# Optimization experiments

Hardware: AMD Instinct MI355X
Metric: run time of the kernel (lower is better)

Reference implementation:

```python
import jax, jax.numpy as jnp
import numpy as np

N = 50000
E = 1600000
HID = 128
H = 8
D = HID // H


def _layer_norm(x, g, b, eps=1e-5):
    mu = jnp.mean(x, axis=-1, keepdims=True)
    var = jnp.mean(jnp.square(x - mu), axis=-1, keepdims=True)
    return (x - mu) * jax.lax.rsqrt(var + eps) * g + b


def setup_inputs() -> dict:
    key = jax.random.key(0)
    ks = jax.random.split(key, 20)
    s = 1.0 / np.sqrt(HID)
    inp = {
        "x": jax.random.normal(ks[0], (N, HID), jnp.float32),
        "edge_index": jax.random.randint(ks[1], (2, E), 0, N, jnp.int64),
        "edge_attr": jax.random.randint(ks[2], (E,), 0, 13, jnp.int64),
        # projections (stored as [in, out] so y = x @ W + b)
        "Wq": jax.random.normal(ks[3], (HID, HID), jnp.float32) * s,
        "bq": jnp.zeros((HID,), jnp.float32),
        "Wk": jax.random.normal(ks[4], (HID, HID), jnp.float32) * s,
        "bk": jnp.zeros((HID,), jnp.float32),
        "Wv": jax.random.normal(ks[5], (HID, HID), jnp.float32) * s,
        "bv": jnp.zeros((HID,), jnp.float32),
        "Wo": jax.random.normal(ks[6], (HID, HID), jnp.float32) * s,
        "bo": jnp.zeros((HID,), jnp.float32),
        "edge_bias_table": jax.random.normal(ks[7], (13, H), jnp.float32) * 0.02,
        "W1": jax.random.normal(ks[8], (HID, 4 * HID), jnp.float32) * s,
        "b1": jnp.zeros((4 * HID,), jnp.float32),
        "W2": jax.random.normal(ks[9], (4 * HID, HID), jnp.float32) * (0.5 * s),
        "b2": jnp.zeros((HID,), jnp.float32),
        "g1": jnp.ones((HID,), jnp.float32),
        "be1": jnp.zeros((HID,), jnp.float32),
        "g2": jnp.ones((HID,), jnp.float32),
        "be2": jnp.zeros((HID,), jnp.float32),
    }
    return inp


def reference(x, edge_index, edge_attr, Wq, bq, Wk, bk, Wv, bv, Wo, bo,
              edge_bias_table, W1, b1, W2, b2, g1, be1, g2, be2):
    n = x.shape[0]
    residual = x
    h = _layer_norm(x, g1, be1)
    Q = (h @ Wq + bq).reshape(n, H, D)
    K = (h @ Wk + bk).reshape(n, H, D)
    V = (h @ Wv + bv).reshape(n, H, D)
    src, dst = edge_index[0], edge_index[1]
    # per-edge scores [E, H]
    scores = jnp.sum(Q[dst] * K[src], axis=-1) / np.sqrt(D)
    scores = scores + edge_bias_table[jnp.clip(edge_attr, 0, 12)]
    # scatter softmax over incoming edges of each dst (global max, as in source)
    scores_exp = jnp.exp(scores - jnp.max(scores))
    attn_sum = jax.ops.segment_sum(scores_exp, dst, num_segments=n)  # [N, H]
    attn_w = scores_exp / (attn_sum[dst] + 1e-8)                      # [E, H]
    messages = V[src] * attn_w[..., None]                             # [E, H, D]
    out = jax.ops.segment_sum(messages, dst, num_segments=n)          # [N, H, D]
    out = out.reshape(n, HID) @ Wo + bo
    x = residual + out  # dropout is identity in eval
    residual = x
    h2 = _layer_norm(x, g2, be2)
    ffn = jax.nn.relu(h2 @ W1 + b1) @ W2 + b2
    return residual + ffn
```

## Files before the change

### kernel.cpp

```cpp
#include <hip/hip_runtime.h>
#include <hip/hip_bf16.h>

#define N_NODES 50000
#define E_EDGES 1600000
#define HID 128
#define NH 8
#define HD 16

#define NBKT 196
#define BKT_CAP 9216
#define CHUNK_A 4096
#define EPT 16
#define BINA_BLOCKS ((E_EDGES + CHUNK_A - 1) / CHUNK_A)
#define WCVT_BLOCKS 771
#define LN_BLOCKS 12500
#define QKV_XBLOCKS ((N_NODES + 127) / 128)
#define ATTN_BLOCKS 2048

using short8 = __attribute__((ext_vector_type(8))) short;
using f32x4  = __attribute__((ext_vector_type(4))) float;
using f32x2  = __attribute__((ext_vector_type(2))) float;
typedef _Float16 h16x2 __attribute__((ext_vector_type(2)));

#if defined(__has_builtin) && __has_builtin(__builtin_amdgcn_fdot2)
#define FDOT2(a, b, c) __builtin_amdgcn_fdot2((a), (b), (c), false)
#else
__device__ __forceinline__ float FDOT2(h16x2 a, h16x2 b, float c) {
    return fmaf((float)a[0], (float)b[0], fmaf((float)a[1], (float)b[1], c));
}
#endif

__device__ __forceinline__ float wave_reduce_sum(float v) {
    #pragma unroll
    for (int off = 32; off > 0; off >>= 1) v += __shfl_xor(v, off, 64);
    return v;
}

__device__ __forceinline__ unsigned int packbf2(float a, float b) {
    __hip_bfloat162 t;
    t.x = __float2bfloat16(a);
    t.y = __float2bfloat16(b);
    unsigned int u;
    __builtin_memcpy(&u, &t, 4);
    return u;
}

__device__ __forceinline__ unsigned char fp8e(float v) {
    return (unsigned char)(__builtin_amdgcn_cvt_pk_fp8_f32(v, v, 0u, false) & 0xFFu);
}

union U4H {
    uint4 u;
    h16x2 h[4];
};

struct KV {
    U4H k0, k1;
    uint4 v;
};

__device__ __forceinline__ KV loadkv(const char* khs, const unsigned char* v8s, unsigned pk) {
    KV r;
    unsigned rr = pk & 0xFFFFu;
    r.k0.u = *(const uint4*)(khs + (rr << 8));
    r.k1.u = *(const uint4*)(khs + (rr << 8) + 16u);
    r.v = *(const uint4*)(v8s + (rr << 7));
    return r;
}

__device__ __forceinline__ void consume_kv(const KV& kv, unsigned pk, bool vd,
                                           const U4H& q0, const U4H& q1,
                                           const float* bLDS, int sub,
                                           f32x2* acc2, float& wsum) {
    float p = 0.f;
    #pragma unroll
    for (int j = 0; j < 4; ++j) p = FDOT2(q0.h[j], kv.k0.h[j], p);
    #pragma unroll
    for (int j = 0; j < 4; ++j) p = FDOT2(q1.h[j], kv.k1.h[j], p);
    float s = p + bLDS[((pk >> 16) & 0xFu) * 8 + sub];
    float w = vd ? __expf(s) : 0.f;
    wsum += w;
    f32x2 w2; w2[0] = w; w2[1] = w;
    f32x2 t;
    t = __builtin_amdgcn_cvt_pk_f32_fp8(kv.v.x, false); acc2[0] = t * w2 + acc2[0];
    t = __builtin_amdgcn_cvt_pk_f32_fp8(kv.v.x, true);  acc2[1] = t * w2 + acc2[1];
    t = __builtin_amdgcn_cvt_pk_f32_fp8(kv.v.y, false); acc2[2] = t * w2 + acc2[2];
    t = __builtin_amdgcn_cvt_pk_f32_fp8(kv.v.y, true);  acc2[3] = t * w2 + acc2[3];
    t = __builtin_amdgcn_cvt_pk_f32_fp8(kv.v.z, false); acc2[4] = t * w2 + acc2[4];
    t = __builtin_amdgcn_cvt_pk_f32_fp8(kv.v.z, true);  acc2[5] = t * w2 + acc2[5];
    t = __builtin_amdgcn_cvt_pk_f32_fp8(kv.v.w, false); acc2[6] = t * w2 + acc2[6];
    t = __builtin_amdgcn_cvt_pk_f32_fp8(kv.v.w, true);  acc2[7] = t * w2 + acc2[7];
}

__global__ __launch_bounds__(256) void prep_kernel(
    const int* __restrict__ ei, const int* __restrict__ attr,
    int* __restrict__ bcur, unsigned int* __restrict__ temp,
    const float* __restrict__ Wq, const float* __restrict__ Wk,
    const float* __restrict__ Wv, const float* __restrict__ Wo,
    const float* __restrict__ W1, const float* __restrict__ W2,
    const float* __restrict__ bq, const float* __restrict__ bk,
    const float* __restrict__ bv,
    __hip_bfloat16* __restrict__ Wqkvt, __hip_bfloat16* __restrict__ Wot,
    __hip_bfloat16* __restrict__ W1t, __hip_bfloat16* __restrict__ W2t,
    float* __restrict__ bqkv,
    const float* __restrict__ x, const float* __restrict__ g1,
    const float* __restrict__ be1, __hip_bfloat16* __restrict__ h_out) {
    __shared__ unsigned int sval[CHUNK_A];
    __shared__ unsigned short sbkt[CHUNK_A];
    __shared__ int hist[NBKT];
    __shared__ int lofs[NBKT];
    __shared__ int gbase[NBKT];
    __shared__ int lcur[NBKT];
    __shared__ int sc[256];
    const int b = blockIdx.x;
    const int tid = threadIdx.x;
    if (b < BINA_BLOCKS) {
        const int e0 = b * CHUNK_A;
        const int n = min(CHUNK_A, E_EDGES - e0);
        for (int i = tid; i < NBKT; i += 256) hist[i] = 0;
        __syncthreads();
        unsigned int v[EPT];
        short bk_[EPT];
        #pragma unroll
        for (int j = 0; j < EPT; ++j) {
            int i = tid + j * 256;
            bk_[j] = -1;
            v[j] = 0;
            if (i < n) {
                int e = e0 + i;
                int src = ei[e];
                int dst = ei[E_EDGES + e];
                int a = attr[e]; a = min(max(a, 0), 12);
                v[j] = (unsigned)src | ((unsigned)a << 16) | ((unsigned)(dst & 255) << 20);
                int bb = dst >> 8;
                bk_[j] = (short)bb;
                atomicAdd(&hist[bb], 1);
            }
        }
        __syncthreads();
        sc[tid] = (tid < NBKT) ? hist[tid] : 0;
        __syncthreads();
        for (int off = 1; off < 256; off <<= 1) {
            int xx = (tid >= off) ? sc[tid - off] : 0;
            __syncthreads();
            sc[tid] += xx;
            __syncthreads();
        }
        if (tid < NBKT) {
            int h = hist[tid];
            lofs[tid] = sc[tid] - h;
            lcur[tid] = 0;
            gbase[tid] = h ? atomicAdd(&bcur[tid], h) : 0;
        }
        __syncthreads();
        #pragma unroll
        for (int j = 0; j < EPT; ++j) {
            if (bk_[j] >= 0) {
                int p = lofs[bk_[j]] + atomicAdd(&lcur[bk_[j]], 1);
                sval[p] = v[j];
                sbkt[p] = (unsigned short)bk_[j];
            }
        }
        __syncthreads();
        for (int i = tid; i < n; i += 256) {
            int bb = sbkt[i];
            temp[(size_t)bb * BKT_CAP + gbase[bb] + (i - lofs[bb])] = sval[i];
        }
    } else if (b < BINA_BLOCKS + WCVT_BLOCKS) {
        int t = (b - BINA_BLOCKS) * 256 + tid;
        if (t >= 196608) {
            int i = t - 196608;
            if (i < 384) bqkv[i] = i < 128 ? bq[i] : (i < 256 ? bk[i - 128] : bv[i - 256]);
            return;
        }
        const float* W; __hip_bfloat16* Wt; int K, N, idx;
        if (t < 65536) {
            int which = t >> 14; idx = t & 16383; K = 128; N = 128;
            W = which == 0 ? Wq : which == 1 ? Wk : which == 2 ? Wv : Wo;
            Wt = which == 3 ? Wot : Wqkvt + which * 16384;
        } else if (t < 131072) { idx = t - 65536;  K = 128; N = 512; W = W1; Wt = W1t; }
        else                   { idx = t - 131072; K = 512; N = 128; W = W2; Wt = W2t; }
        int n = idx / K, k = idx - n * K;
        Wt[idx] = __float2bfloat16(W[(size_t)k * N + n]);
    } else {
        int wave = tid >> 6;
        int lane = tid & 63;
        int row = (b - BINA_BLOCKS - WCVT_BLOCKS) * 4 + wave;
        if (row >= N_NODES) return;
        float2 v = ((const float2*)(x + (size_t)row * HID))[lane];
        float s = wave_reduce_sum(v.x + v.y);
        float mu = s * (1.0f / HID);
        float dx = v.x - mu, dy = v.y - mu;
        float q = wave_reduce_sum(dx * dx + dy * dy);
        float rstd = rsqrtf(q * (1.0f / HID) + 1e-5f);
        float2 gg = ((const float2*)g1)[lane];
        float2 bb = ((const float2*)be1)[lane];
        __hip_bfloat162 o;
        o.x = __float2bfloat16(dx * rstd * gg.x + bb.x);
        o.y = __float2bfloat16(dy * rstd * gg.y + bb.y);
        ((__hip_bfloat162*)(h_out + (size_t)row * HID))[lane] = o;
    }
}

__global__ __launch_bounds__(512) void qkv_binb_kernel(
    const int* __restrict__ bcur, const unsigned int* __restrict__ temp,
    unsigned int* __restrict__ packed, int* __restrict__ offs,
    const __hip_bfloat16* __restrict__ A, const __hip_bfloat16* __restrict__ Wt,
    const float* __restrict__ bias,
    _Float16* __restrict__ Chh, unsigned char* __restrict__ C8, int M) {
    __shared__ short8 smem[2048 + 2048];
    const int tid = threadIdx.x;
    if (blockIdx.x < NBKT) {
        int* cnts = (int*)smem;
        int* hist = cnts + 256;
        int* cur = hist + 256;
        const int b = blockIdx.x;
        if (tid < 256) {
            cnts[tid] = (tid < NBKT) ? bcur[tid] : 0;
            hist[tid] = 0;
        }
        __syncthreads();
        for (int off = 1; off < 256; off <<= 1) {
            int x = 0;
            if (tid < 256 && tid >= off) x = cnts[tid - off];
            __syncthreads();
            if (tid < 256) cnts[tid] += x;
            __syncthreads();
        }
        const int cnt = bcur[b];
        const int start = cnts[b] - cnt;
        const size_t base = (size_t)b * BKT_CAP;
        for (int i = tid; i < cnt; i += 512)
            atomicAdd(&hist[(temp[base + i] >> 20) & 255], 1);
        __syncthreads();
        if (tid < 256) cur[tid] = hist[tid];
        __syncthreads();
        for (int off = 1; off < 256; off <<= 1) {
            int x = 0;
            if (tid < 256 && tid >= off) x = cur[tid - off];
            __syncthreads();
            if (tid < 256) cur[tid] += x;
            __syncthreads();
        }
        const int node0 = b * 256;
        if (tid < 256) {
            int excl = cur[tid] - hist[tid];
            cur[tid] = excl;
            int node = node0 + tid;
            if (node < N_NODES) offs[node] = start + excl;
        }
        if (b == NBKT - 1 && tid == 0) offs[N_NODES] = start + cnt;
        __syncthreads();
        for (int i = tid; i < cnt; i += 512) {
            unsigned int v = temp[base + i];
            int d = (v >> 20) & 255;
            int p = start + atomicAdd(&cur[d], 1);
            packed[p] = v & 0xFFFFFu;
        }
        return;
    }
    const int gb = blockIdx.x - NBKT;
    const int plane = gb / QKV_XBLOCKS;
    const int xb = gb - plane * QKV_XBLOCKS;
    const int row0 = xb * 128;
    const int col0 = plane * 128;
    const int w = tid >> 6, l = tid & 63;
    const int lr = l & 15, hi = l >> 4;
    f32x4 acc[8] = {};
    #pragma unroll
    for (int it = 0; it < 4; ++it) {
        unsigned d = tid + it * 512;
        int r = d >> 4, sd = d & 15;
        int ss = sd ^ (r & 7);
        int gr = row0 + r; if (gr >= M) gr = M - 1;
        __builtin_amdgcn_global_load_lds(
            (const __attribute__((address_space(1))) void*)(A + (size_t)gr * 128 + ss * 8),
            (__attribute__((address_space(3))) void*)(smem + (d & ~63u)),
            16, 0, 0);
    }
    #pragma unroll
    for (int it = 0; it < 4; ++it) {
        unsigned d = tid + it * 512;
        int r = d >> 4, sd = d & 15;
        int ss = sd ^ (r & 7);
        __builtin_amdgcn_global_load_lds(
            (const __attribute__((address_space(1))) void*)(Wt + (size_t)(col0 + r) * 128 + ss * 8),
            (__attribute__((address_space(3))) void*)(smem + 2048 + (d & ~63u)),
            16, 0, 0);
    }
    __syncthreads();
    const int ar = w * 16 + lr;
    #pragma unroll
    for (int ks = 0; ks < 4; ++ks) {
        int s = ks * 4 + hi;
        short8 a = smem[ar * 16 + (s ^ (ar & 7))];
        #pragma unroll
        for (int f = 0; f < 8; ++f) {
            int br = f * 16 + lr;
            short8 b = smem[2048 + br * 16 + (s ^ (br & 7))];
            acc[f] = __builtin_amdgcn_mfma_f32_16x16x32_bf16(a, b, acc[f], 0, 0, 0);
        }
    }
    const float scl = (plane == 0) ? 0.25f : 1.0f;
    #pragma unroll
    for (int f = 0; f < 8; ++f) {
        int c = col0 + f * 16 + lr;
        float bv = bias[c];
        #pragma unroll
        for (int j = 0; j < 4; ++j) {
            int r = row0 + w * 16 + hi * 4 + j;
            if (r < M) {
                float v = acc[f][j] + bv;
                if (plane < 2)
                    Chh[(size_t)plane * N_NODES * 128 + (size_t)r * 128 + (c & 127)] =
                        (_Float16)(v * scl);
                else
                    C8[(size_t)r * 128 + (c & 127)] = fp8e(v);
            }
        }
    }
}

template <int K, int OB>
__global__ __launch_bounds__(512) void gemm_mfma(const __hip_bfloat16* __restrict__ A,
                                                 const __hip_bfloat16* __restrict__ Wt,
                                                 const float* __restrict__ bias,
                                                 const float* __restrict__ res,
                                                 const __hip_bfloat16* __restrict__ resb,
                                                 float* __restrict__ C,
                                                 __hip_bfloat16* __restrict__ Cb,
                                                 __hip_bfloat16* __restrict__ Cx,
                                                 const float* __restrict__ gw,
                                                 const float* __restrict__ bw,
                                                 int M, int NC, int relu) {
    __shared__ short8 smem[2048 + 2048];
    const int row0 = blockIdx.x * 128;
    const int col0 = blockIdx.y * 128;
    const int tid = threadIdx.x;
    const int w = tid >> 6, l = tid & 63;
    const int lr = l & 15, hi = l >> 4;
    f32x4 acc[8] = {};
    for (int kk = 0; kk < K / 128; ++kk) {
        #pragma unroll
        for (int it = 0; it < 4; ++it) {
            unsigned d = tid + it * 512;
            int r = d >> 4, sd = d & 15;
            int ss = sd ^ (r & 7);
            int gr = row0 + r; if (gr >= M) gr = M - 1;
            __builtin_amdgcn_global_load_lds(
                (const __attribute__((address_space(1))) void*)(A + (size_t)gr * K + kk * 128 + ss * 8),
                (__attribute__((address_space(3))) void*)(smem + (d & ~63u)),
                16, 0, 0);
        }
        #pragma unroll
        for (int it = 0; it < 4; ++it) {
            unsigned d = tid + it * 512;
            int r = d >> 4, sd = d & 15;
            int ss = sd ^ (r & 7);
            __builtin_amdgcn_global_load_lds(
                (const __attribute__((address_space(1))) void*)(Wt + (size_t)(col0 + r) * K + kk * 128 + ss * 8),
                (__attribute__((address_space(3))) void*)(smem + 2048 + (d & ~63u)),
                16, 0, 0);
        }
        __syncthreads();
        const int ar = w * 16 + lr;
        #pragma unroll
        for (int ks = 0; ks < 4; ++ks) {
            int s = ks * 4 + hi;
            short8 a = smem[ar * 16 + (s ^ (ar & 7))];
            #pragma unroll
            for (int f = 0; f < 8; ++f) {
                int br = f * 16 + lr;
                short8 b = smem[2048 + br * 16 + (s ^ (br & 7))];
                acc[f] = __builtin_amdgcn_mfma_f32_16x16x32_bf16(a, b, acc[f], 0, 0, 0);
            }
        }
        __syncthreads();
    }
    if (OB == 3) {
        float vv[8][4];
        float gc[8], bc[8];
        #pragma unroll
        for (int f = 0; f < 8; ++f) {
            int c = f * 16 + lr;
            gc[f] = gw[c]; bc[f] = bw[c];
            float bv = bias[c];
            #pragma unroll
            for (int j = 0; j < 4; ++j) {
                int r = row0 + w * 16 + hi * 4 + j;
                int rr = r < M ? r : M - 1;
                vv[f][j] = acc[f][j] + bv + res[(size_t)rr * NC + c];
            }
        }
        #pragma unroll
        for (int j = 0; j < 4; ++j) {
            int r = row0 + w * 16 + hi * 4 + j;
            float s = 0.f, qq = 0.f;
            #pragma unroll
            for (int f = 0; f < 8; ++f) { s += vv[f][j]; qq += vv[f][j] * vv[f][j]; }
            #pragma unroll
            for (int m = 1; m <= 8; m <<= 1) { s += __shfl_xor(s, m); qq += __shfl_xor(qq, m); }
            float mu = s * (1.0f / 128.0f);
            float rstd = rsqrtf(qq * (1.0f / 128.0f) - mu * mu + 1e-5f);
            if (r < M) {
                #pragma unroll
                for (int f = 0; f < 8; ++f) {
                    int c = f * 16 + lr;
                    Cx[(size_t)r * NC + c] = __float2bfloat16(vv[f][j]);
                    Cb[(size_t)r * NC + c] = __float2bfloat16((vv[f][j] - mu) * rstd * gc[f] + bc[f]);
                }
            }
        }
        return;
    }
    #pragma unroll
    for (int f = 0; f < 8; ++f) {
        int c = col0 + f * 16 + lr;
        float bv = bias[c];
        #pragma unroll
        for (int j = 0; j < 4; ++j) {
            int r = row0 + w * 16 + hi * 4 + j;
            if (r < M) {
                float v = acc[f][j] + bv;
                if (relu) v = fmaxf(v, 0.f);
                if (res) v += res[(size_t)r * NC + c];
                if (resb) v += __bfloat162float(resb[(size_t)r * NC + c]);
                if (OB == 0) C[(size_t)r * NC + c] = v;
                else Cb[(size_t)r * NC + c] = __float2bfloat16(v);
            }
        }
    }
}

__global__ __launch_bounds__(256) void fused_attn_kernel(
    const unsigned int* __restrict__ packed,
    const int* __restrict__ offs,
    const _Float16* __restrict__ qkh,
    const unsigned char* __restrict__ v8p,
    const float* __restrict__ btab,
    __hip_bfloat16* __restrict__ out) {
    __shared__ float bLDS[104];
    const int tid = threadIdx.x;
    if (tid < 104) bLDS[tid] = btab[tid];
    __syncthreads();
    const int wave = tid >> 6, lane = tid & 63;
    const int slot = lane >> 3, sub = lane & 7;
    const char* qh = (const char*)qkh;
    const unsigned sb = (unsigned)sub << 5;
    const char* khs = (const char*)(qkh + (size_t)N_NODES * 128) + sb;
    const unsigned char* v8s = v8p + (sb >> 1);
    const unsigned gwave = blockIdx.x * 4 + wave;
    const unsigned stride = ATTN_BLOCKS * 4;
    for (unsigned n = gwave; n < N_NODES; n += stride) {
        U4H q0, q1;
        q0.u = *(const uint4*)(qh + (n << 8) + sb);
        q1.u = *(const uint4*)(qh + (n << 8) + sb + 16u);
        const int lo = offs[n], hi = offs[n + 1];
        const int nit = (hi - lo + 7) >> 3;
        f32x2 acc2[8] = {};
        float wsum = 0.f;
        int i = lo + slot;
        bool vd0 = i < hi;       unsigned pk0 = vd0 ? packed[i] : 0u;
        bool vd1 = i + 8 < hi;   unsigned pk1 = vd1 ? packed[i + 8] : 0u;
        KV a = loadkv(khs, v8s, pk0);
        KV b = loadkv(khs, v8s, pk1);
        int ii = i + 16;
        int rem = nit;
        while (rem >= 2) {
            const bool vd2 = ii < hi;
            const unsigned pk2 = vd2 ? packed[ii] : 0u;
            const bool vd3 = ii + 8 < hi;
            const unsigned pk3 = vd3 ? packed[ii + 8] : 0u;
            consume_kv(a, pk0, vd0, q0, q1, bLDS, sub, acc2, wsum);
            a = loadkv(khs, v8s, pk2);
            consume_kv(b, pk1, vd1, q0, q1, bLDS, sub, acc2, wsum);
            b = loadkv(khs, v8s, pk3);
            pk0 = pk2; vd0 = vd2;
            pk1 = pk3; vd1 = vd3;
            ii += 16;
            rem -= 2;
        }
        if (rem == 1) consume_kv(a, pk0, vd0, q0, q1, bLDS, sub, acc2, wsum);
        float accf[16];
        #pragma unroll
        for (int j = 0; j < 8; ++j) { accf[2 * j] = acc2[j][0]; accf[2 * j + 1] = acc2[j][1]; }
        #pragma unroll
        for (int j = 0; j < 16; ++j) {
            accf[j] += __shfl_xor(accf[j], 8);
            accf[j] += __shfl_xor(accf[j], 16);
            accf[j] += __shfl_xor(accf[j], 32);
        }
        wsum += __shfl_xor(wsum, 8);
        wsum += __shfl_xor(wsum, 16);
        wsum += __shfl_xor(wsum, 32);
        if (slot == 0) {
            float inv = 1.0f / (wsum + 1e-8f);
            uint4 o0, o1;
            o0.x = packbf2(accf[0] * inv, accf[1] * inv);
            o0.y = packbf2(accf[2] * inv, accf[3] * inv);
            o0.z = packbf2(accf[4] * inv, accf[5] * inv);
            o0.w = packbf2(accf[6] * inv, accf[7] * inv);
            o1.x = packbf2(accf[8] * inv, accf[9] * inv);
            o1.y = packbf2(accf[10] * inv, accf[11] * inv);
            o1.z = packbf2(accf[12] * inv, accf[13] * inv);
            o1.w = packbf2(accf[14] * inv, accf[15] * inv);
            char* op = (char*)out + (n << 8) + ((unsigned)sub << 5);
            *(uint4*)op = o0;
            *(uint4*)(op + 16) = o1;
        }
    }
}

extern "C" void kernel_launch(void* const* d_in, const int* in_sizes, int n_in,
                              void* d_out, int out_size, void* d_ws, size_t ws_size,
                              hipStream_t stream) {
    const float* x    = (const float*)d_in[0];
    const int*   ei   = (const int*)d_in[1];
    const int*   attr = (const int*)d_in[2];
    const float* Wq   = (const float*)d_in[3];
    const float* bq   = (const float*)d_in[4];
    const float* Wk   = (const float*)d_in[5];
    const float* bk   = (const float*)d_in[6];
    const float* Wv   = (const float*)d_in[7];
    const float* bv   = (const float*)d_in[8];
    const float* Wo   = (const float*)d_in[9];
    const float* bo   = (const float*)d_in[10];
    const float* ebt  = (const float*)d_in[11];
    const float* W1   = (const float*)d_in[12];
    const float* b1   = (const float*)d_in[13];
    const float* W2   = (const float*)d_in[14];
    const float* b2   = (const float*)d_in[15];
    const float* g1   = (const float*)d_in[16];
    const float* be1  = (const float*)d_in[17];
    const float* g2   = (const float*)d_in[18];
    const float* be2  = (const float*)d_in[19];
    float* out = (float*)d_out;

    char* ws = (char*)d_ws;
    const size_t szRowB = (size_t)N_NODES * HID * 2;
    const size_t ALIGN = 256;
    #define ALN(v) (((v) + ALIGN - 1) & ~(ALIGN - 1))
    size_t o = 0;
    __hip_bfloat16* h_buf = (__hip_bfloat16*)(ws + o); o += szRowB;
    _Float16* QKh = (_Float16*)(ws + o); o += (size_t)N_NODES * 256 * 2;
    unsigned char* V8 = (unsigned char*)(ws + o); o += (size_t)N_NODES * 128;
    unsigned int* packed = (unsigned int*)(ws + o); o += (size_t)E_EDGES * 4;
    unsigned int* temp = (unsigned int*)(ws + o); o += (size_t)NBKT * BKT_CAP * 4;
    int* bcur = (int*)(ws + o); o = ALN(o + (size_t)NBKT * 4);
    int* offs = (int*)(ws + o); o = ALN(o + (size_t)(N_NODES + 1) * 4);
    __hip_bfloat16* attn_ob = (__hip_bfloat16*)(ws + o); o += szRowB;
    __hip_bfloat16* x1b = (__hip_bfloat16*)(ws + o); o += szRowB;
    __hip_bfloat16* f1 = (__hip_bfloat16*)(ws + o); o += (size_t)N_NODES * 512 * 2;
    __hip_bfloat16* Wqkvt = (__hip_bfloat16*)(ws + o); o += 384 * 128 * 2;
    __hip_bfloat16* Wot = (__hip_bfloat16*)(ws + o); o += 128 * 128 * 2;
    __hip_bfloat16* W1t = (__hip_bfloat16*)(ws + o); o += 512 * 128 * 2;
    __hip_bfloat16* W2t = (__hip_bfloat16*)(ws + o); o += 128 * 512 * 2;
    float* bqkv = (float*)(ws + o); o += 384 * 4;
    __hip_bfloat16* h2 = h_buf;

    hipMemsetAsync(bcur, 0, (size_t)NBKT * 4, stream);

    prep_kernel<<<BINA_BLOCKS + WCVT_BLOCKS + LN_BLOCKS, 256, 0, stream>>>(
        ei, attr, bcur, temp,
        Wq, Wk, Wv, Wo, W1, W2, bq, bk, bv,
        Wqkvt, Wot, W1t, W2t, bqkv,
        x, g1, be1, h_buf);

    qkv_binb_kernel<<<NBKT + QKV_XBLOCKS * 3, 512, 0, stream>>>(
        bcur, temp, packed, offs,
        h_buf, Wqkvt, bqkv, QKh, V8, N_NODES);

    fused_attn_kernel<<<ATTN_BLOCKS, 256, 0, stream>>>(packed, offs, QKh, V8, ebt, attn_ob);

    dim3 gm((N_NODES + 127) / 128, 1);
    gemm_mfma<128, 3><<<gm, 512, 0, stream>>>(attn_ob, Wot, bo, x, nullptr,
                                              nullptr, h2, x1b, g2, be2, N_NODES, 128, 0);

    dim3 gf1((N_NODES + 127) / 128, 4);
    gemm_mfma<128, 1><<<gf1, 512, 0, stream>>>(h2, W1t, b1, nullptr, nullptr,
                                               nullptr, f1, nullptr, nullptr, nullptr, N_NODES, 512, 1);
    gemm_mfma<512, 0><<<gm, 512, 0, stream>>>(f1, W2t, b2, nullptr, x1b,
                                              out, nullptr, nullptr, nullptr, nullptr, N_NODES, 128, 0);
}
```

Before: 219.2 us.

## Fuse FFN up- and down-projection GEMMs into one kernel keeping hidden in LDS

Replaces the two FFN GEMM launches (W1 with ReLU writing a 50000x512 bf16 intermediate, then W2 reading it back) with one kernel. Each block handles 32 rows, computes the 512-wide ReLU hidden activations into swizzled LDS, then runs the W2 GEMM directly from LDS and adds the bias and residual. The Wo+LN2 path becomes a specialised non-templated kernel. This removes the global round trip of the intermediate and one launch, but each block now re-reads the full W1/W2 weights for only 32 rows, which costs more sync-heavy serial chunk loops and extra weight traffic.

```diff
diff --git a/kernel.cpp b/kernel.cpp
--- a/kernel.cpp
+++ b/kernel.cpp
@@ -42,6 +42,13 @@
     t.y = __float2bfloat16(b);
     unsigned int u;
     __builtin_memcpy(&u, &t, 4);
+    return u;
+}
+
+__device__ __forceinline__ unsigned short bf16u(float v) {
+    __hip_bfloat16 t = __float2bfloat16(v);
+    unsigned short u;
+    __builtin_memcpy(&u, &t, 2);
     return u;
 }
 
@@ -321,112 +328,193 @@
     }
 }
 
-template <int K, int OB>
-__global__ __launch_bounds__(512) void gemm_mfma(const __hip_bfloat16* __restrict__ A,
-                                                 const __hip_bfloat16* __restrict__ Wt,
-                                                 const float* __restrict__ bias,
-                                                 const float* __restrict__ res,
-                                                 const __hip_bfloat16* __restrict__ resb,
-                                                 float* __restrict__ C,
-                                                 __hip_bfloat16* __restrict__ Cb,
-                                                 __hip_bfloat16* __restrict__ Cx,
-                                                 const float* __restrict__ gw,
-                                                 const float* __restrict__ bw,
-                                                 int M, int NC, int relu) {
+__global__ __launch_bounds__(512) void wo_ln2_kernel(const __hip_bfloat16* __restrict__ A,
+                                                     const __hip_bfloat16* __restrict__ Wt,
+                                                     const float* __restrict__ bias,
+                                                     const float* __restrict__ res,
+                                                     __hip_bfloat16* __restrict__ Cb,
+                                                     __hip_bfloat16* __restrict__ Cx,
+                                                     const float* __restrict__ gw,
+                                                     const float* __restrict__ bw,
+                                                     int M) {
     __shared__ short8 smem[2048 + 2048];
     const int row0 = blockIdx.x * 128;
-    const int col0 = blockIdx.y * 128;
     const int tid = threadIdx.x;
     const int w = tid >> 6, l = tid & 63;
     const int lr = l & 15, hi = l >> 4;
     f32x4 acc[8] = {};
-    for (int kk = 0; kk < K / 128; ++kk) {
+    #pragma unroll
+    for (int it = 0; it < 4; ++it) {
+        unsigned d = tid + it * 512;
+        int r = d >> 4, sd = d & 15;
+        int ss = sd ^ (r & 7);
+        int gr = row0 + r; if (gr >= M) gr = M - 1;
+        __builtin_amdgcn_global_load_lds(
+            (const __attribute__((address_space(1))) void*)(A + (size_t)gr * 128 + ss * 8),
+            (__attribute__((address_space(3))) void*)(smem + (d & ~63u)),
+            16, 0, 0);
+    }
+    #pragma unroll
+    for (int it = 0; it < 4; ++it) {
+        unsigned d = tid + it * 512;
+        int r = d >> 4, sd = d & 15;
+        int ss = sd ^ (r & 7);
+        __builtin_amdgcn_global_load_lds(
+            (const __attribute__((address_space(1))) void*)(Wt + (size_t)r * 128 + ss * 8),
+            (__attribute__((address_space(3))) void*)(smem + 2048 + (d & ~63u)),
+            16, 0, 0);
+    }
+    __syncthreads();
+    const int ar = w * 16 + lr;
+    #pragma unroll
+    for (int ks = 0; ks < 4; ++ks) {
+        int s = ks * 4 + hi;
+        short8 a = smem[ar * 16 + (s ^ (ar & 7))];
+        #pragma unroll
+        for (int f = 0; f < 8; ++f) {
+            int br = f * 16 + lr;
+            short8 b = smem[2048 + br * 16 + (s ^ (br & 7))];
+            acc[f] = __builtin_amdgcn_mfma_f32_16x16x32_bf16(a, b, acc[f], 0, 0, 0);
+        }
+    }
+    float vv[8][4];
+    float gc[8], bc[8];
+    #pragma unroll
+    for (int f = 0; f < 8; ++f) {
+        int c = f * 16 + lr;
+        gc[f] = gw[c]; bc[f] = bw[c];
+        float bv = bias[c];
+        #pragma unroll
+        for (int j = 0; j < 4; ++j) {
+            int r = row0 + w * 16 + hi * 4 + j;
+            int rr = r < M ? r : M - 1;
+            vv[f][j] = acc[f][j] + bv + res[(size_t)rr * 128 + c];
+        }
+    }
+    #pragma unroll
+    for (int j = 0; j < 4; ++j) {
+        int r = row0 + w * 16 + hi * 4 + j;
+        float s = 0.f, qq = 0.f;
+        #pragma unroll
+        for (int f = 0; f < 8; ++f) { s += vv[f][j]; qq += vv[f][j] * vv[f][j]; }
+        #pragma unroll
+        for (int m = 1; m <= 8; m <<= 1) { s += __shfl_xor(s, m); qq += __shfl_xor(qq, m); }
+        float mu = s * (1.0f / 128.0f);
+        float rstd = rsqrtf(qq * (1.0f / 128.0f) - mu * mu + 1e-5f);
+        if (r < M) {
+            #pragma unroll
+            for (int f = 0; f < 8; ++f) {
+                int c = f * 16 + lr;
+                Cx[(size_t)r * 128 + c] = __float2bfloat16(vv[f][j]);
+                Cb[(size_t)r * 128 + c] = __float2bfloat16((vv[f][j] - mu) * rstd * gc[f] + bc[f]);
+            }
+        }
+    }
+}
+
+__global__ __launch_bounds__(256) void ffn_fused_kernel(
+    const __hip_bfloat16* __restrict__ h2,
+    const __hip_bfloat16* __restrict__ W1t,
+    const float* __restrict__ b1,
+    const __hip_bfloat16* __restrict__ W2t,
+    const float* __restrict__ b2,
+    const __hip_bfloat16* __restrict__ x1b,
+    float* __restrict__ outp, int M) {
+    __shared__ short8 aLDS[512];
+    __shared__ short8 bLDS[1024];
+    __shared__ unsigned short fLDS[32 * 512];
+    const int tid = threadIdx.x;
+    const int row0 = blockIdx.x * 32;
+    const int w = tid >> 6, l = tid & 63;
+    const int lr = l & 15, hi = l >> 4;
+    const int rt = w & 1, ch = w >> 1;
+    #pragma unroll
+    for (int it = 0; it < 2; ++it) {
+        unsigned d = tid + it * 256;
+        int r = d >> 4, sd = d & 15;
+        int ss = sd ^ (r & 7);
+        int gr = row0 + r; if (gr >= M) gr = M - 1;
+        __builtin_amdgcn_global_load_lds(
+            (const __attribute__((address_space(1))) void*)(h2 + (size_t)gr * 128 + ss * 8),
+            (__attribute__((address_space(3))) void*)(aLDS + (d & ~63u)),
+            16, 0, 0);
+    }
+    const int ar = rt * 16 + lr;
+    for (int cc = 0; cc < 8; ++cc) {
         #pragma unroll
         for (int it = 0; it < 4; ++it) {
-            unsigned d = tid + it * 512;
-            int r = d >> 4, sd = d & 15;
-            int ss = sd ^ (r & 7);
-            int gr = row0 + r; if (gr >= M) gr = M - 1;
+            unsigned d = tid + it * 256;
+            int rb = d >> 4, sd = d & 15;
+            int ss = sd ^ (rb & 7);
             __builtin_amdgcn_global_load_lds(
-                (const __attribute__((address_space(1))) void*)(A + (size_t)gr * K + kk * 128 + ss * 8),
-                (__attribute__((address_space(3))) void*)(smem + (d & ~63u)),
+                (const __attribute__((address_space(1))) void*)(W1t + (size_t)(cc * 64 + rb) * 128 + ss * 8),
+                (__attribute__((address_space(3))) void*)(bLDS + (d & ~63u)),
                 16, 0, 0);
         }
-        #pragma unroll
-        for (int it = 0; it < 4; ++it) {
-            unsigned d = tid + it * 512;
-            int r = d >> 4, sd = d & 15;
-            int ss = sd ^ (r & 7);
-            __builtin_amdgcn_global_load_lds(
-                (const __attribute__((address_space(1))) void*)(Wt + (size_t)(col0 + r) * K + kk * 128 + ss * 8),
-                (__attribute__((address_space(3))) void*)(smem + 2048 + (d & ~63u)),
-                16, 0, 0);
-        }
-        __syncthreads();
-        const int ar = w * 16 + lr;
+        __syncthreads();
+        f32x4 acc0 = {}, acc1 = {};
         #pragma unroll
         for (int ks = 0; ks < 4; ++ks) {
             int s = ks * 4 + hi;
-            short8 a = smem[ar * 16 + (s ^ (ar & 7))];
-            #pragma unroll
-            for (int f = 0; f < 8; ++f) {
-                int br = f * 16 + lr;
-                short8 b = smem[2048 + br * 16 + (s ^ (br & 7))];
-                acc[f] = __builtin_amdgcn_mfma_f32_16x16x32_bf16(a, b, acc[f], 0, 0, 0);
-            }
-        }
-        __syncthreads();
-    }
-    if (OB == 3) {
-        float vv[8][4];
-        float gc[8], bc[8];
-        #pragma unroll
-        for (int f = 0; f < 8; ++f) {
-            int c = f * 16 + lr;
-            gc[f] = gw[c]; bc[f] = bw[c];
-            float bv = bias[c];
+            short8 a = aLDS[ar * 16 + (s ^ (ar & 7))];
+            int rb0 = ch * 32 + lr;
+            short8 b0 = bLDS[rb0 * 16 + (s ^ (rb0 & 7))];
+            acc0 = __builtin_amdgcn_mfma_f32_16x16x32_bf16(a, b0, acc0, 0, 0, 0);
+            int rb1 = ch * 32 + 16 + lr;
+            short8 b1v = bLDS[rb1 * 16 + (s ^ (rb1 & 7))];
+            acc1 = __builtin_amdgcn_mfma_f32_16x16x32_bf16(a, b1v, acc1, 0, 0, 0);
+        }
+        #pragma unroll
+        for (int f = 0; f < 2; ++f) {
+            int c = cc * 64 + ch * 32 + f * 16 + lr;
+            float bv = b1[c];
+            int seg = c >> 3;
             #pragma unroll
             for (int j = 0; j < 4; ++j) {
-                int r = row0 + w * 16 + hi * 4 + j;
-                int rr = r < M ? r : M - 1;
-                vv[f][j] = acc[f][j] + bv + res[(size_t)rr * NC + c];
+                int r = rt * 16 + hi * 4 + j;
+                float v = fmaxf((f == 0 ? acc0[j] : acc1[j]) + bv, 0.f);
+                fLDS[r * 512 + ((seg ^ (r & 7)) << 3) + (c & 7)] = bf16u(v);
             }
         }
+        __syncthreads();
+    }
+    f32x4 acc2[4] = {};
+    for (int kc = 0; kc < 8; ++kc) {
+        #pragma unroll
+        for (int it = 0; it < 4; ++it) {
+            unsigned d = tid + it * 256;
+            int rb = d >> 3, sd = d & 7;
+            int ss = sd ^ (rb & 7);
+            __builtin_amdgcn_global_load_lds(
+                (const __attribute__((address_space(1))) void*)(W2t + (size_t)rb * 512 + kc * 64 + ss * 8),
+                (__attribute__((address_space(3))) void*)(bLDS + (d & ~63u)),
+                16, 0, 0);
+        }
+        __syncthreads();
+        #pragma unroll
+        for (int ks = 0; ks < 2; ++ks) {
+            int ksg = kc * 8 + ks * 4 + hi;
+            short8 a = *(const short8*)&fLDS[ar * 512 + ((ksg ^ (ar & 7)) << 3)];
+            int s2 = ks * 4 + hi;
+            #pragma unroll
+            for (int f = 0; f < 4; ++f) {
+                int rb = ch * 64 + f * 16 + lr;
+                short8 b = bLDS[rb * 8 + (s2 ^ (rb & 7))];
+                acc2[f] = __builtin_amdgcn_mfma_f32_16x16x32_bf16(a, b, acc2[f], 0, 0, 0);
+            }
+        }
+        __syncthreads();
+    }
+    #pragma unroll
+    for (int f = 0; f < 4; ++f) {
+        int c = ch * 64 + f * 16 + lr;
+        float bv = b2[c];
         #pragma unroll
         for (int j = 0; j < 4; ++j) {
-            int r = row0 + w * 16 + hi * 4 + j;
-            float s = 0.f, qq = 0.f;
-            #pragma unroll
-            for (int f = 0; f < 8; ++f) { s += vv[f][j]; qq += vv[f][j] * vv[f][j]; }
-            #pragma unroll
-            for (int m = 1; m <= 8; m <<= 1) { s += __shfl_xor(s, m); qq += __shfl_xor(qq, m); }
-            float mu = s * (1.0f / 128.0f);
-            float rstd = rsqrtf(qq * (1.0f / 128.0f) - mu * mu + 1e-5f);
+            int r = row0 + rt * 16 + hi * 4 + j;
             if (r < M) {
-                #pragma unroll
-                for (int f = 0; f < 8; ++f) {
-                    int c = f * 16 + lr;
-                    Cx[(size_t)r * NC + c] = __float2bfloat16(vv[f][j]);
-                    Cb[(size_t)r * NC + c] = __float2bfloat16((vv[f][j] - mu) * rstd * gc[f] + bc[f]);
-                }
-            }
-        }
-        return;
-    }
-    #pragma unroll
-    for (int f = 0; f < 8; ++f) {
-        int c = col0 + f * 16 + lr;
-        float bv = bias[c];
-        #pragma unroll
-        for (int j = 0; j < 4; ++j) {
-            int r = row0 + w * 16 + hi * 4 + j;
-            if (r < M) {
-                float v = acc[f][j] + bv;
-                if (relu) v = fmaxf(v, 0.f);
-                if (res) v += res[(size_t)r * NC + c];
-                if (resb) v += __bfloat162float(resb[(size_t)r * NC + c]);
-                if (OB == 0) C[(size_t)r * NC + c] = v;
-                else Cb[(size_t)r * NC + c] = __float2bfloat16(v);
+                float v = acc2[f][j] + bv + __bfloat162float(x1b[(size_t)r * 128 + c]);
+                outp[(size_t)r * 128 + c] = v;
             }
         }
     }
@@ -550,7 +638,6 @@
     int* offs = (int*)(ws + o); o = ALN(o + (size_t)(N_NODES + 1) * 4);
     __hip_bfloat16* attn_ob = (__hip_bfloat16*)(ws + o); o += szRowB;
     __hip_bfloat16* x1b = (__hip_bfloat16*)(ws + o); o += szRowB;
-    __hip_bfloat16* f1 = (__hip_bfloat16*)(ws + o); o += (size_t)N_NODES * 512 * 2;
     __hip_bfloat16* Wqkvt = (__hip_bfloat16*)(ws + o); o += 384 * 128 * 2;
     __hip_bfloat16* Wot = (__hip_bfloat16*)(ws + o); o += 128 * 128 * 2;
     __hip_bfloat16* W1t = (__hip_bfloat16*)(ws + o); o += 512 * 128 * 2;
@@ -572,13 +659,9 @@
 
     fused_attn_kernel<<<ATTN_BLOCKS, 256, 0, stream>>>(packed, offs, QKh, V8, ebt, attn_ob);
 
-    dim3 gm((N_NODES + 127) / 128, 1);
-    gemm_mfma<128, 3><<<gm, 512, 0, stream>>>(attn_ob, Wot, bo, x, nullptr,
-                                              nullptr, h2, x1b, g2, be2, N_NODES, 128, 0);
-
-    dim3 gf1((N_NODES + 127) / 128, 4);
-    gemm_mfma<128, 1><<<gf1, 512, 0, stream>>>(h2, W1t, b1, nullptr, nullptr,
-                                               nullptr, f1, nullptr, nullptr, nullptr, N_NODES, 512, 1);
-    gemm_mfma<512, 0><<<gm, 512, 0, stream>>>(f1, W2t, b2, nullptr, x1b,
-                                              out, nullptr, nullptr, nullptr, nullptr, N_NODES, 128, 0);
-}
+    wo_ln2_kernel<<<(N_NODES + 127) / 128, 512, 0, stream>>>(
+        attn_ob, Wot, bo, x, h2, x1b, g2, be2, N_NODES);
+
+    ffn_fused_kernel<<<(N_NODES + 31) / 32, 256, 0, stream>>>(
+        h2, W1t, b1, W2t, b2, x1b, out, N_NODES);
+}
```

New measurement: 208.2 us. -5.0%, faster.
